# Kernel tuning notes

Hardware: AMD Instinct MI355X
Metric: run time of the kernel (lower is better)

## Reference

```python
import jax, jax.numpy as jnp
import numpy as np

DIM = 256        # data dimension D
NUM_ATOMS = 512  # codebook size K
N_COLS = 65536   # number of signal columns (batch*H*W flattened)


def setup_inputs() -> dict:
    key = jax.random.key(0)
    k1, k2 = jax.random.split(key)
    z_e = jax.random.normal(k1, (DIM, N_COLS), dtype=jnp.float32)
    # learned parameter: nn.Parameter(torch.randn(num_atoms, dim))
    dictionary = jax.random.normal(k2, (NUM_ATOMS, DIM), dtype=jnp.float32)
    return {"z_e": z_e, "dictionary": dictionary}


def reference(z_e, dictionary):
    """Faithful JAX version of DictionaryLearningOMP.forward.

    The torch loop recomputes sparse_code = pinv(D) @ X on EVERY iteration
    (it never restricts to the selected atoms I), so sparse_code is constant
    across iterations: at iteration 2 the reconstruction distance between
    cur and last sparse codes is exactly 0 < epsilon and the loop stops.
    The argmax atom indices I are never used in the returned value, so the
    forward output is exactly (pinv(D) @ X).T.
    """
    D = dictionary.T                      # [dim, K]
    X = z_e.reshape(D.shape[0], -1)       # [dim, N]
    Dpinv = jnp.linalg.pinv(D)            # [K, dim]
    sparse_code = Dpinv @ X               # [K, N]
    return sparse_code.T                  # [N, K]
```

## Files before the change

### kernel.cpp

```cpp
#include <hip/hip_runtime.h>

typedef short  s16x8 __attribute__((ext_vector_type(8)));
typedef float  f32x4 __attribute__((ext_vector_type(4)));

#define NCOL 65536
#define DIMV 256
#define KATOMS 512

#define LAM_LO 25.0f
#define LAM_HI 1650.0f
#define C0 (2.0f / (LAM_LO + LAM_HI))

static __device__ __forceinline__ unsigned short f2bf(float x) {
  unsigned u = __float_as_uint(x);
  u += 0x7fffu + ((u >> 16) & 1u);
  return (unsigned short)(u >> 16);
}

__global__ __launch_bounds__(1024) void gram_init(const float* __restrict__ dict,
                                                  float* __restrict__ G,
                                                  float* __restrict__ X) {
  __shared__ float S0[KATOMS];
  __shared__ float Pp[4][DIMV];
  const int tid = threadIdx.x;
  const int r = blockIdx.x;
  if (tid < KATOMS) S0[tid] = dict[(size_t)tid * DIMV + r];
  __syncthreads();
  const int c = tid & 255, ks = tid >> 8;
  {
    float acc = 0.f;
    const int k0 = ks * 128;
#pragma unroll 8
    for (int k = 0; k < 128; ++k)
      acc += S0[k0 + k] * dict[(size_t)(k0 + k) * DIMV + c];
    Pp[ks][c] = acc;
  }
  __syncthreads();
  if (tid < 256) {
    const float g = ((Pp[0][c] + Pp[1][c]) + Pp[2][c]) + Pp[3][c];
    G[(size_t)r * DIMV + c] = g;
    X[(size_t)r * DIMV + c] = (r == c ? 2.f * C0 : 0.f) - C0 * C0 * g;
  }
}

__global__ __launch_bounds__(1024) void ns_iter(const float* __restrict__ G,
                                                const float* __restrict__ Xin,
                                                float* __restrict__ Xout,
                                                float a, float b) {
  __shared__ float S1[DIMV], Ps[DIMV];
  __shared__ float Pp[4][DIMV];
  const int tid = threadIdx.x;
  const int r = blockIdx.x;
  if (tid < 256) S1[tid] = Xin[(size_t)r * DIMV + tid];
  __syncthreads();
  const int c = tid & 255, ks = tid >> 8;
  const int k0 = ks * 64;
  {
    float p = 0.f;
#pragma unroll 8
    for (int k = 0; k < 64; ++k)
      p += S1[k0 + k] * G[(size_t)(k0 + k) * DIMV + c];
    Pp[ks][c] = p;
  }
  __syncthreads();
  if (tid < 256) Ps[c] = ((Pp[0][c] + Pp[1][c]) + Pp[2][c]) + Pp[3][c];
  __syncthreads();
  {
    float q = 0.f;
#pragma unroll 8
    for (int k = 0; k < 64; ++k)
      q += Ps[k0 + k] * Xin[(size_t)(k0 + k) * DIMV + c];
    Pp[ks][c] = q;
  }
  __syncthreads();
  if (tid < 256) {
    const float q = ((Pp[0][c] + Pp[1][c]) + Pp[2][c]) + Pp[3][c];
    Xout[(size_t)r * DIMV + c] = a * S1[c] - b * q;
  }
}

__global__ __launch_bounds__(1024) void make_m(const float* __restrict__ dict,
                                               const float* __restrict__ X,
                                               unsigned short* __restrict__ Mb) {
  __shared__ float S1[DIMV], S2[DIMV];
  __shared__ float Qp0[4][DIMV], Qp1[4][DIMV];
  const int tid = threadIdx.x;
  const int r = blockIdx.x;
  if (tid < 256) {
    S1[tid] = dict[(size_t)r * DIMV + tid];
    S2[tid] = dict[(size_t)(r + 256) * DIMV + tid];
  }
  __syncthreads();
  const int c = tid & 255, ks = tid >> 8;
  const int k0 = ks * 64;
  {
    float q0 = 0.f, q1 = 0.f;
#pragma unroll 8
    for (int k = 0; k < 64; ++k) {
      const float xv = X[(size_t)(k0 + k) * DIMV + c];
      q0 += S1[k0 + k] * xv;
      q1 += S2[k0 + k] * xv;
    }
    Qp0[ks][c] = q0;
    Qp1[ks][c] = q1;
  }
  __syncthreads();
  if (tid < 256) {
    const float q0 = ((Qp0[0][c] + Qp0[1][c]) + Qp0[2][c]) + Qp0[3][c];
    const float q1 = ((Qp1[0][c] + Qp1[1][c]) + Qp1[2][c]) + Qp1[3][c];
    Mb[(size_t)r * DIMV + c] = f2bf(q0);
    Mb[(size_t)(r + 256) * DIMV + c] = f2bf(q1);
  }
}

__global__ __launch_bounds__(512, 2) void big_gemm(const float* __restrict__ z,
                                                   const unsigned short* __restrict__ Mb,
                                                   float* __restrict__ out) {
  __shared__ unsigned int lds_w[64 * 132];
  const int tid = threadIdx.x;
  const int l = tid & 63, w = tid >> 6;
  const int mm = l & 15, q = l >> 4;
  const unsigned short* lds_s = (const unsigned short*)lds_w;

  s16x8 b[32];
#pragma unroll
  for (int dstep = 0; dstep < 8; ++dstep)
#pragma unroll
    for (int s = 0; s < 4; ++s)
      b[dstep * 4 + s] = *(const s16x8*)(Mb + (size_t)(w * 64 + mm * 4 + s) * DIMV +
                                         dstep * 32 + 8 * q);

#pragma unroll 1
  for (int t = 0; t < 2; ++t) {
    const int n0 = blockIdx.x * 128 + t * 64;
    __syncthreads();

    {
      const int nq = tid & 15, dpb = tid >> 4;
#pragma unroll
      for (int i = 0; i < 4; ++i) {
        const int dp = i * 32 + dpb;
        const float* zp = z + (size_t)(2 * dp) * NCOL + n0 + 4 * nq;
        const f32x4 r0 = *(const f32x4*)zp;
        const f32x4 r1 = *(const f32x4*)(zp + NCOL);
#pragma unroll
        for (int j = 0; j < 4; ++j)
          lds_w[(4 * nq + j) * 132 + dp] =
              (unsigned)f2bf(r0[j]) | ((unsigned)f2bf(r1[j]) << 16);
      }
    }
    __syncthreads();

    f32x4 acc[4][4];
#pragma unroll
    for (int ns = 0; ns < 4; ++ns)
#pragma unroll
      for (int s = 0; s < 4; ++s) acc[ns][s] = (f32x4){0.f, 0.f, 0.f, 0.f};

#pragma unroll
    for (int dstep = 0; dstep < 8; ++dstep) {
      s16x8 a[4];
#pragma unroll
      for (int ns = 0; ns < 4; ++ns)
        a[ns] = *(const s16x8*)(lds_s + (size_t)(ns * 16 + mm) * 264 + dstep * 32 + 8 * q);
#pragma unroll
      for (int ns = 0; ns < 4; ++ns)
#pragma unroll
        for (int s = 0; s < 4; ++s)
          acc[ns][s] = __builtin_amdgcn_mfma_f32_16x16x32_bf16(a[ns], b[dstep * 4 + s],
                                                               acc[ns][s], 0, 0, 0);
    }

#pragma unroll
    for (int ns = 0; ns < 4; ++ns)
#pragma unroll
      for (int r = 0; r < 4; ++r) {
        const int row = n0 + ns * 16 + 4 * q + r;
        const int col0 = w * 64 + mm * 4;
        f32x4 v = (f32x4){acc[ns][0][r], acc[ns][1][r], acc[ns][2][r], acc[ns][3][r]};
        *(f32x4*)(out + (size_t)row * KATOMS + col0) = v;
      }
  }
}

extern "C" void kernel_launch(void* const* d_in, const int* in_sizes, int n_in,
                              void* d_out, int out_size, void* d_ws, size_t ws_size,
                              hipStream_t stream) {
  const float* z    = (const float*)d_in[0];
  const float* dict = (const float*)d_in[1];
  float* out = (float*)d_out;

  const size_t MAT = (size_t)DIMV * DIMV;
  float* tail = out + (size_t)out_size - 3 * MAT;
  float* G  = tail;
  float* Xa = tail + MAT;
  float* Xb = tail + 2 * MAT;
  unsigned short* Mb = (unsigned short*)d_ws;

  gram_init<<<256, 1024, 0, stream>>>(dict, G, Xa);

  const double gammas[6] = {1.888912, 1.653116, 1.271098, 1.038134, 1.000731, 1.0};
  float* Xc = Xa;
  float* Xn = Xb;
  for (int it = 0; it < 6; ++it) {
    const float g = (float)gammas[it];
    ns_iter<<<256, 1024, 0, stream>>>(G, Xc, Xn, 2.f * g, g * g);
    float* tmp = Xc; Xc = Xn; Xn = tmp;
  }

  make_m<<<256, 1024, 0, stream>>>(dict, Xc, Mb);

  big_gemm<<<NCOL / 128, 512, 0, stream>>>(z, Mb, out);
}
```

Measured before the change: 255.8 us.

## Fuse Gram, Newton-Schulz iterations and M build into one persistent kernel

Replaces the eight small launches (Gram init, six Newton-Schulz iterations, make_m) with a single 64-block persistent kernel that uses atomic-counter grid barriers between phases. Each block now handles four rows (eight for M), so every load of G or X from global memory is reused across several rows. This removes per-launch overhead and inter-kernel gaps on the serial preprocessing chain. The cost is spin-wait barriers, lower parallelism (64 blocks instead of 256), an extra memset, and a reliance on all 64 blocks being co-resident.

```diff
diff --git a/kernel.cpp b/kernel.cpp
--- a/kernel.cpp
+++ b/kernel.cpp
@@ -6,6 +6,7 @@
 #define NCOL 65536
 #define DIMV 256
 #define KATOMS 512
+#define PBLK 64
 
 #define LAM_LO 25.0f
 #define LAM_HI 1650.0f
@@ -17,99 +18,121 @@
   return (unsigned short)(u >> 16);
 }
 
-__global__ __launch_bounds__(1024) void gram_init(const float* __restrict__ dict,
-                                                  float* __restrict__ G,
-                                                  float* __restrict__ X) {
-  __shared__ float S0[KATOMS];
-  __shared__ float Pp[4][DIMV];
+static __device__ __forceinline__ void gbar(unsigned* cnt, unsigned nblk) {
+  __syncthreads();
+  if (threadIdx.x == 0) {
+    __threadfence();
+    __hip_atomic_fetch_add(cnt, 1u, __ATOMIC_RELEASE, __HIP_MEMORY_SCOPE_AGENT);
+    while (__hip_atomic_load(cnt, __ATOMIC_ACQUIRE, __HIP_MEMORY_SCOPE_AGENT) < nblk)
+      __builtin_amdgcn_s_sleep(2);
+    __threadfence();
+  }
+  __syncthreads();
+}
+
+__global__ __launch_bounds__(1024) void prep_chain(
+    const float* __restrict__ dict, float* __restrict__ G,
+    float* __restrict__ Xa, float* __restrict__ Xb,
+    unsigned short* __restrict__ Mb, unsigned* __restrict__ cnt) {
+  __shared__ f32x4 SC4[KATOMS];
+  __shared__ float SX[4][DIMV];
+  __shared__ float Pp[4][4][DIMV];
+  __shared__ float Ps[4][DIMV];
+  __shared__ float SD[8][DIMV];
+  __shared__ float Qp[4][8][DIMV];
   const int tid = threadIdx.x;
-  const int r = blockIdx.x;
-  if (tid < KATOMS) S0[tid] = dict[(size_t)tid * DIMV + r];
-  __syncthreads();
+  const int b = blockIdx.x;
   const int c = tid & 255, ks = tid >> 8;
-  {
-    float acc = 0.f;
+
+  if (tid < KATOMS)
+    SC4[tid] = *(const f32x4*)(dict + (size_t)tid * DIMV + 4 * b);
+  __syncthreads();
+  {
     const int k0 = ks * 128;
-#pragma unroll 8
-    for (int k = 0; k < 128; ++k)
-      acc += S0[k0 + k] * dict[(size_t)(k0 + k) * DIMV + c];
-    Pp[ks][c] = acc;
-  }
-  __syncthreads();
-  if (tid < 256) {
-    const float g = ((Pp[0][c] + Pp[1][c]) + Pp[2][c]) + Pp[3][c];
+    float a0 = 0.f, a1 = 0.f, a2 = 0.f, a3 = 0.f;
+#pragma unroll 8
+    for (int k = 0; k < 128; ++k) {
+      const f32x4 col = SC4[k0 + k];
+      const float dv = dict[(size_t)(k0 + k) * DIMV + c];
+      a0 += col[0] * dv; a1 += col[1] * dv; a2 += col[2] * dv; a3 += col[3] * dv;
+    }
+    Pp[ks][0][c] = a0; Pp[ks][1][c] = a1; Pp[ks][2][c] = a2; Pp[ks][3][c] = a3;
+  }
+  __syncthreads();
+  {
+    const int j = ks;
+    const int r = 4 * b + j;
+    const float g = ((Pp[0][j][c] + Pp[1][j][c]) + Pp[2][j][c]) + Pp[3][j][c];
     G[(size_t)r * DIMV + c] = g;
-    X[(size_t)r * DIMV + c] = (r == c ? 2.f * C0 : 0.f) - C0 * C0 * g;
-  }
-}
-
-__global__ __launch_bounds__(1024) void ns_iter(const float* __restrict__ G,
-                                                const float* __restrict__ Xin,
-                                                float* __restrict__ Xout,
-                                                float a, float b) {
-  __shared__ float S1[DIMV], Ps[DIMV];
-  __shared__ float Pp[4][DIMV];
-  const int tid = threadIdx.x;
-  const int r = blockIdx.x;
-  if (tid < 256) S1[tid] = Xin[(size_t)r * DIMV + tid];
-  __syncthreads();
-  const int c = tid & 255, ks = tid >> 8;
-  const int k0 = ks * 64;
-  {
-    float p = 0.f;
-#pragma unroll 8
-    for (int k = 0; k < 64; ++k)
-      p += S1[k0 + k] * G[(size_t)(k0 + k) * DIMV + c];
-    Pp[ks][c] = p;
-  }
-  __syncthreads();
-  if (tid < 256) Ps[c] = ((Pp[0][c] + Pp[1][c]) + Pp[2][c]) + Pp[3][c];
-  __syncthreads();
-  {
-    float q = 0.f;
-#pragma unroll 8
-    for (int k = 0; k < 64; ++k)
-      q += Ps[k0 + k] * Xin[(size_t)(k0 + k) * DIMV + c];
-    Pp[ks][c] = q;
-  }
-  __syncthreads();
-  if (tid < 256) {
-    const float q = ((Pp[0][c] + Pp[1][c]) + Pp[2][c]) + Pp[3][c];
-    Xout[(size_t)r * DIMV + c] = a * S1[c] - b * q;
-  }
-}
-
-__global__ __launch_bounds__(1024) void make_m(const float* __restrict__ dict,
-                                               const float* __restrict__ X,
-                                               unsigned short* __restrict__ Mb) {
-  __shared__ float S1[DIMV], S2[DIMV];
-  __shared__ float Qp0[4][DIMV], Qp1[4][DIMV];
-  const int tid = threadIdx.x;
-  const int r = blockIdx.x;
-  if (tid < 256) {
-    S1[tid] = dict[(size_t)r * DIMV + tid];
-    S2[tid] = dict[(size_t)(r + 256) * DIMV + tid];
-  }
-  __syncthreads();
-  const int c = tid & 255, ks = tid >> 8;
-  const int k0 = ks * 64;
-  {
-    float q0 = 0.f, q1 = 0.f;
+    Xa[(size_t)r * DIMV + c] = (r == c ? 2.f * C0 : 0.f) - C0 * C0 * g;
+  }
+  gbar(cnt + 0, PBLK);
+
+  const float gam[6] = {1.888912f, 1.653116f, 1.271098f, 1.038134f, 1.000731f, 1.0f};
+  float* Xc = Xa;
+  float* Xn = Xb;
+#pragma unroll 1
+  for (int it = 0; it < 6; ++it) {
+    const float g = gam[it];
+    const float a = 2.f * g, bb = g * g;
+    SX[ks][c] = Xc[(size_t)(4 * b + ks) * DIMV + c];
+    __syncthreads();
+    const int k0 = ks * 64;
+    {
+      float p0 = 0.f, p1 = 0.f, p2 = 0.f, p3 = 0.f;
+#pragma unroll 8
+      for (int k = 0; k < 64; ++k) {
+        const float gv = G[(size_t)(k0 + k) * DIMV + c];
+        p0 += SX[0][k0 + k] * gv; p1 += SX[1][k0 + k] * gv;
+        p2 += SX[2][k0 + k] * gv; p3 += SX[3][k0 + k] * gv;
+      }
+      Pp[ks][0][c] = p0; Pp[ks][1][c] = p1; Pp[ks][2][c] = p2; Pp[ks][3][c] = p3;
+    }
+    __syncthreads();
+    Ps[ks][c] = ((Pp[0][ks][c] + Pp[1][ks][c]) + Pp[2][ks][c]) + Pp[3][ks][c];
+    __syncthreads();
+    {
+      float q0 = 0.f, q1 = 0.f, q2 = 0.f, q3 = 0.f;
+#pragma unroll 8
+      for (int k = 0; k < 64; ++k) {
+        const float xv = Xc[(size_t)(k0 + k) * DIMV + c];
+        q0 += Ps[0][k0 + k] * xv; q1 += Ps[1][k0 + k] * xv;
+        q2 += Ps[2][k0 + k] * xv; q3 += Ps[3][k0 + k] * xv;
+      }
+      Pp[ks][0][c] = q0; Pp[ks][1][c] = q1; Pp[ks][2][c] = q2; Pp[ks][3][c] = q3;
+    }
+    __syncthreads();
+    {
+      const int j = ks;
+      const float q = ((Pp[0][j][c] + Pp[1][j][c]) + Pp[2][j][c]) + Pp[3][j][c];
+      Xn[(size_t)(4 * b + j) * DIMV + c] = a * SX[j][c] - bb * q;
+    }
+    float* tmp = Xc; Xc = Xn; Xn = tmp;
+    gbar(cnt + 1 + it, PBLK);
+  }
+
+  SD[ks][c]     = dict[(size_t)(8 * b + ks) * DIMV + c];
+  SD[ks + 4][c] = dict[(size_t)(8 * b + ks + 4) * DIMV + c];
+  __syncthreads();
+  {
+    const int k0 = ks * 64;
+    float q[8] = {0.f, 0.f, 0.f, 0.f, 0.f, 0.f, 0.f, 0.f};
 #pragma unroll 8
     for (int k = 0; k < 64; ++k) {
-      const float xv = X[(size_t)(k0 + k) * DIMV + c];
-      q0 += S1[k0 + k] * xv;
-      q1 += S2[k0 + k] * xv;
-    }
-    Qp0[ks][c] = q0;
-    Qp1[ks][c] = q1;
-  }
-  __syncthreads();
-  if (tid < 256) {
-    const float q0 = ((Qp0[0][c] + Qp0[1][c]) + Qp0[2][c]) + Qp0[3][c];
-    const float q1 = ((Qp1[0][c] + Qp1[1][c]) + Qp1[2][c]) + Qp1[3][c];
-    Mb[(size_t)r * DIMV + c] = f2bf(q0);
-    Mb[(size_t)(r + 256) * DIMV + c] = f2bf(q1);
+      const float xv = Xc[(size_t)(k0 + k) * DIMV + c];
+#pragma unroll
+      for (int j = 0; j < 8; ++j) q[j] += SD[j][k0 + k] * xv;
+    }
+#pragma unroll
+    for (int j = 0; j < 8; ++j) Qp[ks][j][c] = q[j];
+  }
+  __syncthreads();
+  {
+    const int j = ks;
+    const float qa = ((Qp[0][j][c] + Qp[1][j][c]) + Qp[2][j][c]) + Qp[3][j][c];
+    const float qb = ((Qp[0][j + 4][c] + Qp[1][j + 4][c]) + Qp[2][j + 4][c]) + Qp[3][j + 4][c];
+    Mb[(size_t)(8 * b + j) * DIMV + c] = f2bf(qa);
+    Mb[(size_t)(8 * b + j + 4) * DIMV + c] = f2bf(qb);
   }
 }
 
@@ -191,24 +214,16 @@
   float* out = (float*)d_out;
 
   const size_t MAT = (size_t)DIMV * DIMV;
-  float* tail = out + (size_t)out_size - 3 * MAT;
+  float* tail = out + (size_t)out_size - 3 * MAT - 64;
   float* G  = tail;
   float* Xa = tail + MAT;
   float* Xb = tail + 2 * MAT;
+  unsigned* cnt = (unsigned*)(tail + 3 * MAT);
   unsigned short* Mb = (unsigned short*)d_ws;
 
-  gram_init<<<256, 1024, 0, stream>>>(dict, G, Xa);
-
-  const double gammas[6] = {1.888912, 1.653116, 1.271098, 1.038134, 1.000731, 1.0};
-  float* Xc = Xa;
-  float* Xn = Xb;
-  for (int it = 0; it < 6; ++it) {
-    const float g = (float)gammas[it];
-    ns_iter<<<256, 1024, 0, stream>>>(G, Xc, Xn, 2.f * g, g * g);
-    float* tmp = Xc; Xc = Xn; Xn = tmp;
-  }
-
-  make_m<<<256, 1024, 0, stream>>>(dict, Xc, Mb);
+  hipMemsetAsync(cnt, 0, 64 * sizeof(float), stream);
+
+  prep_chain<<<PBLK, 1024, 0, stream>>>(dict, G, Xa, Xb, Mb, cnt);
 
   big_gemm<<<NCOL / 128, 512, 0, stream>>>(z, Mb, out);
 }
```

Measured after the change: 297.0 us. +16.1%, slower.
